# Kernel tuning notes

Hardware: AMD Instinct MI355X
Metric: run time of the kernel (lower is better)

## Reference

```python
import jax, jax.numpy as jnp
import numpy as np


def _segsum(x):
    """Stable segment-sum. x: (..., l) -> (..., l, l) lower-triangular sums."""
    l = x.shape[-1]
    cs = jnp.cumsum(x, axis=-1)
    seg = cs[..., :, None] - cs[..., None, :]
    mask = jnp.tril(jnp.ones((l, l), dtype=bool))
    return jnp.where(mask, seg, -jnp.inf)


def setup_inputs() -> dict:
    key = jax.random.key(0)
    kx, ka, kb, kc = jax.random.split(key, 4)
    b, s, h, p, n = 4, 8192, 32, 64, 16
    X = jax.random.normal(kx, (b, s, h, p), dtype=jnp.float32)
    # negative A for realistic decaying SSM dynamics / numerical safety
    A = -jnp.abs(jax.random.normal(ka, (b, s, h), dtype=jnp.float32)) * 0.5
    B = jax.random.normal(kb, (b, s, h, n), dtype=jnp.float32)
    C = jax.random.normal(kc, (b, s, h, n), dtype=jnp.float32)
    return {"X": X, "A": A, "B": B, "C": C, "block_len": 64}


def reference(X, A, B, C, block_len):
    b, s, h, p = X.shape
    n = B.shape[-1]
    c = s // block_len
    l = block_len
    # chunk: (b, c, l, ...)
    Xb = X.reshape(b, c, l, h, p)
    Bb = B.reshape(b, c, l, h, n)
    Cb = C.reshape(b, c, l, h, n)
    Ab = A.reshape(b, c, l, h).transpose(0, 3, 1, 2)  # (b, h, c, l)
    A_cumsum = jnp.cumsum(Ab, axis=-1)                # (b, h, c, l)

    # 1) intra-chunk (diagonal) output
    L = jnp.exp(_segsum(Ab))                          # (b, h, c, l, l)
    Y_diag = jnp.einsum("bclhn,bcshn,bhcls,bcshp->bclhp", Cb, Bb, L, Xb)

    # 2) intra-chunk states (chunk-final state contribution)
    decay_states = jnp.exp(A_cumsum[..., -1:] - A_cumsum)   # (b, h, c, l)
    states = jnp.einsum("bclhn,bhcl,bclhp->bchpn", Bb, decay_states, Xb)

    # 3) inter-chunk recurrence (zero initial states)
    A_last = A_cumsum[..., -1]                        # (b, h, c)
    decay_chunk = jnp.exp(_segsum(jnp.pad(A_last, ((0, 0), (0, 0), (1, 0)))))  # (b,h,c+1,c+1)
    states = jnp.concatenate([jnp.zeros_like(states[:, :1]), states], axis=1)  # (b,c+1,h,p,n)
    new_states = jnp.einsum("bhzc,bchpn->bzhpn", decay_chunk, states)
    states = new_states[:, :-1]                       # states entering each chunk

    # 4) state -> output (off-diagonal)
    state_decay_out = jnp.exp(A_cumsum)               # (b, h, c, l)
    Y_off = jnp.einsum("bclhn,bchpn,bhcl->bclhp", Cb, states, state_decay_out)

    Y = (Y_diag + Y_off).reshape(b, s, h, p)
    return Y
```

## Files before the change

kernel.cpp:

```cpp
#include <hip/hip_runtime.h>

#define BB 4
#define SS 8192
#define HH 32
#define PP 64
#define NN 16
#define LL 64
#define CC 128
#define SEG 4
#define NSEG (CC / SEG)
#define NCHAIN (BB * HH)
#define NSEGT (NCHAIN * NSEG)

typedef __attribute__((ext_vector_type(8))) short bf16x8;
typedef __attribute__((ext_vector_type(4))) float f32x4;

__device__ inline short f2bf(float f) {
    unsigned u = __builtin_bit_cast(unsigned, f);
    u = (u + 0x7FFFu + ((u >> 16) & 1u)) >> 16;
    return (short)u;
}

__global__ __launch_bounds__(256) void k1_carries(
    const float* __restrict__ X, const float* __restrict__ A,
    const float* __restrict__ B, float* __restrict__ carry,
    float* __restrict__ segd)
{
    int seg = blockIdx.x;
    int chain = seg >> 5;
    int kseg = seg & (NSEG - 1);
    int h = chain & (HH - 1);
    int b = chain >> 5;
    int tid = threadIdx.x;
    int w = tid >> 6, l = tid & 63, g = l >> 4, lr = l & 15;

    __shared__ float Bs[2][LL][17];
    __shared__ float csL[2][LL];
    __shared__ float wls[2][LL];

    float P[4] = {0.f, 0.f, 0.f, 0.f};
    float asum = 0.f;
    float xr[16]; float4 br; float ar = 0.f;

    int c0 = kseg * SEG;

    auto LOADS = [&](int c) {
        size_t row0 = (size_t)b * SS + (size_t)c * LL;
        const float* Xp = X + (row0 * HH + h) * PP;
        const float* Bp = B + (row0 * HH + h) * NN;
        const float* Ap = A + row0 * HH + h;
#pragma unroll
        for (int kt = 0; kt < 2; ++kt)
#pragma unroll
            for (int e = 0; e < 8; ++e)
                xr[kt * 8 + e] = Xp[(size_t)(kt * 32 + g * 8 + e) * (HH * PP) + 16 * w + lr];
        br = *(const float4*)(Bp + (size_t)(tid >> 2) * (HH * NN) + (tid & 3) * 4);
        if (tid < 64) ar = Ap[(size_t)tid * HH];
    };

    auto WRITE = [&](int q1) {
        if (tid < 64) {
            float x = ar;
#pragma unroll
            for (int d = 1; d < 64; d <<= 1) {
                float t = __shfl_up(x, d, 64);
                if (tid >= d) x += t;
            }
            csL[q1][tid] = x;
            float al2 = __shfl(x, 63, 64);
            wls[q1][tid] = __expf(al2 - x);
        }
        int r = tid >> 2, qq = tid & 3;
        Bs[q1][r][qq * 4 + 0] = br.x;
        Bs[q1][r][qq * 4 + 1] = br.y;
        Bs[q1][r][qq * 4 + 2] = br.z;
        Bs[q1][r][qq * 4 + 3] = br.w;
    };

    LOADS(c0);
    WRITE(0);
    __syncthreads();

    for (int cc = 0; cc < SEG; ++cc) {
        int q = cc & 1;
        bf16x8 xf0, xf1;
#pragma unroll
        for (int e = 0; e < 8; ++e) { xf0[e] = f2bf(xr[e]); xf1[e] = f2bf(xr[8 + e]); }
        if (cc + 1 < SEG) LOADS(c0 + cc + 1);

        bf16x8 bt[2];
#pragma unroll
        for (int kt = 0; kt < 2; ++kt) {
            bf16x8 t;
#pragma unroll
            for (int e = 0; e < 8; ++e) {
                int ll2 = kt * 32 + g * 8 + e;
                t[e] = f2bf(Bs[q][ll2][lr] * wls[q][ll2]);
            }
            bt[kt] = t;
        }
        f32x4 st = __builtin_amdgcn_mfma_f32_16x16x32_bf16(bt[0], xf0, (f32x4)0.f, 0, 0, 0);
        st = __builtin_amdgcn_mfma_f32_16x16x32_bf16(bt[1], xf1, st, 0, 0, 0);

        float alast = csL[q][LL - 1];
        float ea = __expf(alast);
#pragma unroll
        for (int r = 0; r < 4; ++r) P[r] = ea * P[r] + st[r];
        asum += alast;

        if (cc + 1 < SEG) WRITE(q ^ 1);
        __syncthreads();
    }

    float4 pv = {P[0], P[1], P[2], P[3]};
    *(float4*)(carry + (size_t)seg * (PP * NN) + (16 * w + lr) * NN + 4 * g) = pv;
    if (tid == 0) segd[seg] = asum;
}

__global__ __launch_bounds__(256) void k2_scan(
    const float* __restrict__ carry, const float* __restrict__ segd,
    float* __restrict__ pin)
{
    int chain = blockIdx.x >> 2;
    int t = ((blockIdx.x & 3) << 8) + threadIdx.x;
    const float* cb = carry + (size_t)chain * NSEG * (PP * NN) + t;
    float* pb = pin + (size_t)chain * NSEG * (PP * NN) + t;
    const float* as = segd + chain * NSEG;
    float P = 0.f;
    for (int k0 = 0; k0 < NSEG; k0 += 8) {
        float s[8], av[8], o[8];
#pragma unroll
        for (int u = 0; u < 8; ++u) s[u] = cb[(size_t)(k0 + u) * (PP * NN)];
#pragma unroll
        for (int u = 0; u < 8; ++u) av[u] = as[k0 + u];
#pragma unroll
        for (int u = 0; u < 8; ++u) { o[u] = P; P = __expf(av[u]) * P + s[u]; }
#pragma unroll
        for (int u = 0; u < 8; ++u) pb[(size_t)(k0 + u) * (PP * NN)] = o[u];
    }
}

__global__ __launch_bounds__(256) void k3_y(
    const float* __restrict__ X, const float* __restrict__ A,
    const float* __restrict__ Bm, const float* __restrict__ Cm,
    const float* __restrict__ pin, float* __restrict__ Y)
{
    int seg = blockIdx.x;
    int chain = seg >> 5;
    int kseg = seg & (NSEG - 1);
    int h = chain & (HH - 1);
    int b = chain >> 5;
    int tid = threadIdx.x;
    int w = tid >> 6, l = tid & 63, g = l >> 4, lr = l & 15;

    __shared__ short XTF[2][8 * 64 * 8];
    __shared__ short ScF[8 * 64 * 8];
    __shared__ float Bs[2][LL][17];
    __shared__ short PT16[2][NN * 68];
    __shared__ float csL[2][LL];
    __shared__ float wls[2][LL];

    ((bf16x8*)ScF)[tid] = (bf16x8)0;
    ((bf16x8*)ScF)[tid + 256] = (bf16x8)0;

    float4 pv = *(const float4*)(pin + (size_t)seg * (PP * NN) + (16 * w + lr) * NN + 4 * g);
    float P[4] = {pv.x, pv.y, pv.z, pv.w};

    float xr[16]; float4 br, cr0, cr1; float ar = 0.f;
    bf16x8 caw;

    int c0 = kseg * SEG;

    auto LOADS = [&](int c) {
        size_t row0 = (size_t)b * SS + (size_t)c * LL;
        const float* Xp = X + (row0 * HH + h) * PP;
        const float* Bp = Bm + (row0 * HH + h) * NN;
        const float* Cp = Cm + (row0 * HH + h) * NN;
        const float* Ap = A + row0 * HH + h;
#pragma unroll
        for (int si = 0; si < 2; ++si) {
            int s = tid + si * 256;
            int sl = s & 63, pt = (s >> 6) & 3, kt = s >> 8;
            int pp2 = pt * 16 + (sl & 15);
            int k0 = kt * 32 + (sl >> 4) * 8;
#pragma unroll
            for (int e = 0; e < 8; ++e)
                xr[si * 8 + e] = Xp[(size_t)(k0 + e) * (HH * PP) + pp2];
        }
        br = *(const float4*)(Bp + (size_t)(tid >> 2) * (HH * NN) + (tid & 3) * 4);
        if (g < 2) {
            const float* crp = Cp + (size_t)(16 * w + lr) * (HH * NN) + g * 8;
            cr0 = *(const float4*)crp;
            cr1 = *(const float4*)(crp + 4);
        }
        if (tid < 64) ar = Ap[(size_t)tid * HH];
    };

    auto WRITE = [&](int q1) {
        if (tid < 64) {
            float x = ar;
#pragma unroll
            for (int d = 1; d < 64; d <<= 1) {
                float t = __shfl_up(x, d, 64);
                if (tid >= d) x += t;
            }
            csL[q1][tid] = x;
            float al2 = __shfl(x, 63, 64);
            wls[q1][tid] = __expf(al2 - x);
        }
        {
            int r = tid >> 2, qq = tid & 3;
            Bs[q1][r][qq * 4 + 0] = br.x;
            Bs[q1][r][qq * 4 + 1] = br.y;
            Bs[q1][r][qq * 4 + 2] = br.z;
            Bs[q1][r][qq * 4 + 3] = br.w;
        }
#pragma unroll
        for (int si = 0; si < 2; ++si) {
            int s = tid + si * 256;
            bf16x8 xb;
#pragma unroll
            for (int e = 0; e < 8; ++e) xb[e] = f2bf(xr[si * 8 + e]);
            ((bf16x8*)(XTF[q1]))[s] = xb;
        }
#pragma unroll
        for (int r = 0; r < 4; ++r)
            PT16[q1][(4 * g + r) * 68 + 16 * w + lr] = f2bf(P[r]);
        bf16x8 t = (bf16x8)0;
        if (g < 2) {
            t[0] = f2bf(cr0.x); t[1] = f2bf(cr0.y); t[2] = f2bf(cr0.z); t[3] = f2bf(cr0.w);
            t[4] = f2bf(cr1.x); t[5] = f2bf(cr1.y); t[6] = f2bf(cr1.z); t[7] = f2bf(cr1.w);
        }
        caw = t;
    };

    LOADS(c0);
    WRITE(0);
    __syncthreads();

    for (int cc = 0; cc < SEG; ++cc) {
        int q = cc & 1;
        if (cc + 1 < SEG) LOADS(c0 + cc + 1);

        float alast = csL[q][LL - 1];
        float cs_i[4], ei[4];
        int ib = 16 * w + 4 * g;
#pragma unroll
        for (int r = 0; r < 4; ++r) { cs_i[r] = csL[q][ib + r]; ei[r] = __expf(cs_i[r]); }

        bf16x8 pf[4];
#pragma unroll
        for (int pt = 0; pt < 4; ++pt) {
            bf16x8 t = (bf16x8)0;
            if (g < 2) {
#pragma unroll
                for (int e = 0; e < 8; ++e)
                    t[e] = PT16[q][(g * 8 + e) * 68 + pt * 16 + lr];
            }
            pf[pt] = t;
        }
        bf16x8 bt[2];
#pragma unroll
        for (int kt = 0; kt < 2; ++kt) {
            bf16x8 t;
#pragma unroll
            for (int e = 0; e < 8; ++e) {
                int ll2 = kt * 32 + g * 8 + e;
                t[e] = f2bf(Bs[q][ll2][lr] * wls[q][ll2]);
            }
            bt[kt] = t;
        }

        for (int jt = 0; jt <= w; ++jt) {
            bf16x8 bw = (bf16x8)0;
            if (g < 2) {
#pragma unroll
                for (int e = 0; e < 8; ++e)
                    bw[e] = f2bf(Bs[q][jt * 16 + lr][g * 8 + e]);
            }
            f32x4 sr = __builtin_amdgcn_mfma_f32_16x16x32_bf16(caw, bw, (f32x4)0.f, 0, 0, 0);
            int j = jt * 16 + lr;
            float csj = csL[q][j];
            int kt2 = j >> 5;
            int flb = 16 * ((j >> 3) & 3);
#pragma unroll
            for (int r = 0; r < 4; ++r) {
                int i15 = g * 4 + r;
                int i = 16 * w + i15;
                float v = (j <= i) ? sr[r] * __expf(cs_i[r] - csj) : 0.f;
                ScF[((w * 2 + kt2) * 64 + i15 + flb) * 8 + (j & 7)] = f2bf(v);
            }
        }

        f32x4 acc[4];
#pragma unroll
        for (int pt = 0; pt < 4; ++pt)
            acc[pt] = __builtin_amdgcn_mfma_f32_16x16x32_bf16(caw, pf[pt], (f32x4)0.f, 0, 0, 0);
#pragma unroll
        for (int pt = 0; pt < 4; ++pt)
#pragma unroll
            for (int r = 0; r < 4; ++r) acc[pt][r] *= ei[r];

        int kts = (w >= 2) ? 2 : 1;
        for (int kt = 0; kt < kts; ++kt) {
            bf16x8 af = ((bf16x8*)ScF)[(w * 2 + kt) * 64 + l];
#pragma unroll
            for (int pt = 0; pt < 4; ++pt) {
                bf16x8 xf = ((bf16x8*)(XTF[q]))[(kt * 4 + pt) * 64 + l];
                acc[pt] = __builtin_amdgcn_mfma_f32_16x16x32_bf16(af, xf, acc[pt], 0, 0, 0);
            }
        }

        f32x4 st = (f32x4)0.f;
#pragma unroll
        for (int kt = 0; kt < 2; ++kt) {
            bf16x8 xf = ((bf16x8*)(XTF[q]))[(kt * 4 + w) * 64 + l];
            st = __builtin_amdgcn_mfma_f32_16x16x32_bf16(bt[kt], xf, st, 0, 0, 0);
        }
        float ea = __expf(alast);
#pragma unroll
        for (int r = 0; r < 4; ++r) P[r] = ea * P[r] + st[r];

        {
            size_t row0 = (size_t)b * SS + (size_t)(c0 + cc) * LL;
            float* Yp = Y + (row0 * HH + h) * PP;
#pragma unroll
            for (int pt = 0; pt < 4; ++pt)
#pragma unroll
                for (int r = 0; r < 4; ++r)
                    Yp[(size_t)(16 * w + 4 * g + r) * (HH * PP) + pt * 16 + lr] = acc[pt][r];
        }

        if (cc + 1 < SEG) WRITE(q ^ 1);
        __syncthreads();
    }
}

extern "C" void kernel_launch(void* const* d_in, const int* in_sizes, int n_in,
                              void* d_out, int out_size, void* d_ws, size_t ws_size,
                              hipStream_t stream)
{
    const float* X = (const float*)d_in[0];
    const float* A = (const float*)d_in[1];
    const float* B = (const float*)d_in[2];
    const float* C = (const float*)d_in[3];
    float* Y = (float*)d_out;

    float* carry = (float*)d_ws;
    float* pin   = carry + (size_t)NSEGT * (PP * NN);
    float* segd  = pin   + (size_t)NSEGT * (PP * NN);

    dim3 blk(256);
    k1_carries<<<dim3(NSEGT), blk, 0, stream>>>(X, A, B, carry, segd);
    k2_scan<<<dim3(NCHAIN * 4), blk, 0, stream>>>(carry, segd, pin);
    k3_y<<<dim3(NSEGT), blk, 0, stream>>>(X, A, B, C, pin, Y);
}
```

Measured before the change: 286.4 us.

## Parallelize output kernel per chunk using stored intra-segment partial states

Result: faster. 275.9 us (-3.7%).

```diff
diff --git a/kernel.cpp b/kernel.cpp
--- a/kernel.cpp
+++ b/kernel.cpp
@@ -11,8 +11,10 @@
 #define NSEG (CC / SEG)
 #define NCHAIN (BB * HH)
 #define NSEGT (NCHAIN * NSEG)
+#define NCHT (NCHAIN * CC)
 
 typedef __attribute__((ext_vector_type(8))) short bf16x8;
+typedef __attribute__((ext_vector_type(4))) short bf16x4;
 typedef __attribute__((ext_vector_type(4))) float f32x4;
 
 __device__ inline short f2bf(float f) {
@@ -24,7 +26,8 @@
 __global__ __launch_bounds__(256) void k1_carries(
     const float* __restrict__ X, const float* __restrict__ A,
     const float* __restrict__ B, float* __restrict__ carry,
-    float* __restrict__ segd)
+    float* __restrict__ segd, float* __restrict__ ploc,
+    float* __restrict__ dsum)
 {
     int seg = blockIdx.x;
     int chain = seg >> 5;
@@ -43,6 +46,7 @@
     float xr[16]; float4 br; float ar = 0.f;
 
     int c0 = kseg * SEG;
+    int pnoff = (16 * w + lr) * NN + 4 * g;
 
     auto LOADS = [&](int c) {
         size_t row0 = (size_t)b * SS + (size_t)c * LL;
@@ -83,6 +87,11 @@
 
     for (int cc = 0; cc < SEG; ++cc) {
         int q = cc & 1;
+        if (cc > 0) {
+            float4 pv = {P[0], P[1], P[2], P[3]};
+            *(float4*)(ploc + (size_t)(chain * CC + c0 + cc) * (PP * NN) + pnoff) = pv;
+            if (tid == 0) dsum[chain * CC + c0 + cc] = asum;
+        }
         bf16x8 xf0, xf1;
 #pragma unroll
         for (int e = 0; e < 8; ++e) { xf0[e] = f2bf(xr[e]); xf1[e] = f2bf(xr[8 + e]); }
@@ -113,7 +122,7 @@
     }
 
     float4 pv = {P[0], P[1], P[2], P[3]};
-    *(float4*)(carry + (size_t)seg * (PP * NN) + (16 * w + lr) * NN + 4 * g) = pv;
+    *(float4*)(carry + (size_t)seg * (PP * NN) + pnoff) = pv;
     if (tid == 0) segd[seg] = asum;
 }
 
@@ -143,197 +152,153 @@
 __global__ __launch_bounds__(256) void k3_y(
     const float* __restrict__ X, const float* __restrict__ A,
     const float* __restrict__ Bm, const float* __restrict__ Cm,
-    const float* __restrict__ pin, float* __restrict__ Y)
+    const float* __restrict__ pin, const float* __restrict__ ploc,
+    const float* __restrict__ dsum, float* __restrict__ Y)
 {
-    int seg = blockIdx.x;
-    int chain = seg >> 5;
-    int kseg = seg & (NSEG - 1);
-    int h = chain & (HH - 1);
-    int b = chain >> 5;
+    int blk = blockIdx.x;
+    int h = blk & (HH - 1);
+    int c = (blk >> 5) & (CC - 1);
+    int b = blk >> 12;
     int tid = threadIdx.x;
     int w = tid >> 6, l = tid & 63, g = l >> 4, lr = l & 15;
-
-    __shared__ short XTF[2][8 * 64 * 8];
+    int chain = b * HH + h;
+    int seg = chain * NSEG + (c >> 2);
+
+    __shared__ short XTF[8 * 64 * 8];
     __shared__ short ScF[8 * 64 * 8];
-    __shared__ float Bs[2][LL][17];
-    __shared__ short PT16[2][NN * 68];
-    __shared__ float csL[2][LL];
-    __shared__ float wls[2][LL];
+    __shared__ short BsF[4 * 64 * 8];
+    __shared__ short PF[4 * 64 * 8];
+    __shared__ float csL[LL];
+
+    size_t row0 = (size_t)b * SS + (size_t)c * LL;
+    const float* Xp = X + (row0 * HH + h) * PP;
+    const float* Bp = Bm + (row0 * HH + h) * NN;
+    const float* Cp = Cm + (row0 * HH + h) * NN;
+    const float* Ap = A + row0 * HH + h;
+    float* Yp = Y + (row0 * HH + h) * PP;
+
+    float xr[16];
+#pragma unroll
+    for (int si = 0; si < 2; ++si) {
+        int k0 = si * 32 + g * 8;
+#pragma unroll
+        for (int e = 0; e < 8; ++e)
+            xr[si * 8 + e] = Xp[(size_t)(k0 + e) * (HH * PP) + 16 * w + lr];
+    }
+    int r = tid >> 2, q = tid & 3;
+    float4 br = *(const float4*)(Bp + (size_t)r * (HH * NN) + q * 4);
+    float4 cr0 = {0,0,0,0}, cr1 = {0,0,0,0};
+    if (g < 2) {
+        const float* crp = Cp + (size_t)(16 * w + lr) * (HH * NN) + g * 8;
+        cr0 = *(const float4*)crp;
+        cr1 = *(const float4*)(crp + 4);
+    }
+    float ar = 0.f;
+    if (tid < 64) ar = Ap[(size_t)tid * HH];
+    int pnoff = (16 * w + lr) * NN + 4 * g;
+    float4 pinv = *(const float4*)(pin + (size_t)seg * (PP * NN) + pnoff);
+    float P4[4];
+    if ((c & (SEG - 1)) == 0) {
+        P4[0] = pinv.x; P4[1] = pinv.y; P4[2] = pinv.z; P4[3] = pinv.w;
+    } else {
+        float4 plv = *(const float4*)(ploc + (size_t)(chain * CC + c) * (PP * NN) + pnoff);
+        float ed = __expf(dsum[chain * CC + c]);
+        P4[0] = ed * pinv.x + plv.x;
+        P4[1] = ed * pinv.y + plv.y;
+        P4[2] = ed * pinv.z + plv.z;
+        P4[3] = ed * pinv.w + plv.w;
+    }
 
     ((bf16x8*)ScF)[tid] = (bf16x8)0;
     ((bf16x8*)ScF)[tid + 256] = (bf16x8)0;
-
-    float4 pv = *(const float4*)(pin + (size_t)seg * (PP * NN) + (16 * w + lr) * NN + 4 * g);
-    float P[4] = {pv.x, pv.y, pv.z, pv.w};
-
-    float xr[16]; float4 br, cr0, cr1; float ar = 0.f;
-    bf16x8 caw;
-
-    int c0 = kseg * SEG;
-
-    auto LOADS = [&](int c) {
-        size_t row0 = (size_t)b * SS + (size_t)c * LL;
-        const float* Xp = X + (row0 * HH + h) * PP;
-        const float* Bp = Bm + (row0 * HH + h) * NN;
-        const float* Cp = Cm + (row0 * HH + h) * NN;
-        const float* Ap = A + row0 * HH + h;
-#pragma unroll
-        for (int si = 0; si < 2; ++si) {
-            int s = tid + si * 256;
-            int sl = s & 63, pt = (s >> 6) & 3, kt = s >> 8;
-            int pp2 = pt * 16 + (sl & 15);
-            int k0 = kt * 32 + (sl >> 4) * 8;
-#pragma unroll
-            for (int e = 0; e < 8; ++e)
-                xr[si * 8 + e] = Xp[(size_t)(k0 + e) * (HH * PP) + pp2];
-        }
-        br = *(const float4*)(Bp + (size_t)(tid >> 2) * (HH * NN) + (tid & 3) * 4);
-        if (g < 2) {
-            const float* crp = Cp + (size_t)(16 * w + lr) * (HH * NN) + g * 8;
-            cr0 = *(const float4*)crp;
-            cr1 = *(const float4*)(crp + 4);
-        }
-        if (tid < 64) ar = Ap[(size_t)tid * HH];
-    };
-
-    auto WRITE = [&](int q1) {
-        if (tid < 64) {
-            float x = ar;
-#pragma unroll
-            for (int d = 1; d < 64; d <<= 1) {
-                float t = __shfl_up(x, d, 64);
-                if (tid >= d) x += t;
-            }
-            csL[q1][tid] = x;
-            float al2 = __shfl(x, 63, 64);
-            wls[q1][tid] = __expf(al2 - x);
-        }
-        {
-            int r = tid >> 2, qq = tid & 3;
-            Bs[q1][r][qq * 4 + 0] = br.x;
-            Bs[q1][r][qq * 4 + 1] = br.y;
-            Bs[q1][r][qq * 4 + 2] = br.z;
-            Bs[q1][r][qq * 4 + 3] = br.w;
-        }
-#pragma unroll
-        for (int si = 0; si < 2; ++si) {
-            int s = tid + si * 256;
-            bf16x8 xb;
-#pragma unroll
-            for (int e = 0; e < 8; ++e) xb[e] = f2bf(xr[si * 8 + e]);
-            ((bf16x8*)(XTF[q1]))[s] = xb;
-        }
-#pragma unroll
-        for (int r = 0; r < 4; ++r)
-            PT16[q1][(4 * g + r) * 68 + 16 * w + lr] = f2bf(P[r]);
-        bf16x8 t = (bf16x8)0;
-        if (g < 2) {
-            t[0] = f2bf(cr0.x); t[1] = f2bf(cr0.y); t[2] = f2bf(cr0.z); t[3] = f2bf(cr0.w);
-            t[4] = f2bf(cr1.x); t[5] = f2bf(cr1.y); t[6] = f2bf(cr1.z); t[7] = f2bf(cr1.w);
-        }
-        caw = t;
-    };
-
-    LOADS(c0);
-    WRITE(0);
+    if (tid < 128)
+        ((bf16x8*)PF)[(tid >> 5) * 64 + 32 + (tid & 31)] = (bf16x8)0;
+
+#pragma unroll
+    for (int si = 0; si < 2; ++si) {
+        bf16x8 xb;
+#pragma unroll
+        for (int e = 0; e < 8; ++e) xb[e] = f2bf(xr[si * 8 + e]);
+        ((bf16x8*)XTF)[tid + si * 256] = xb;
+    }
+    {
+        int fl = (r & 15) + 16 * (q >> 1);
+        int jt = r >> 4;
+        bf16x4 bb = { f2bf(br.x), f2bf(br.y), f2bf(br.z), f2bf(br.w) };
+        ((bf16x4*)BsF)[(jt * 64 + fl) * 2 + (q & 1)] = bb;
+        int zt = tid >> 6, zu = (tid >> 1) & 31, zv = tid & 1;
+        ((bf16x4*)BsF)[(zt * 64 + 32 + zu) * 2 + zv] = (bf16x4)0;
+    }
+#pragma unroll
+    for (int rr = 0; rr < 4; ++rr) {
+        int n = 4 * g + rr;
+        PF[(w * 64 + (n >> 3) * 16 + lr) * 8 + (n & 7)] = f2bf(P4[rr]);
+    }
+    bf16x8 caw = (bf16x8)0;
+    if (g < 2) {
+        caw[0] = f2bf(cr0.x); caw[1] = f2bf(cr0.y);
+        caw[2] = f2bf(cr0.z); caw[3] = f2bf(cr0.w);
+        caw[4] = f2bf(cr1.x); caw[5] = f2bf(cr1.y);
+        caw[6] = f2bf(cr1.z); caw[7] = f2bf(cr1.w);
+    }
+    if (tid < 64) {
+        float x = ar;
+#pragma unroll
+        for (int d = 1; d < 64; d <<= 1) {
+            float t = __shfl_up(x, d, 64);
+            if (tid >= d) x += t;
+        }
+        csL[tid] = x;
+    }
     __syncthreads();
 
-    for (int cc = 0; cc < SEG; ++cc) {
-        int q = cc & 1;
-        if (cc + 1 < SEG) LOADS(c0 + cc + 1);
-
-        float alast = csL[q][LL - 1];
-        float cs_i[4], ei[4];
-        int ib = 16 * w + 4 * g;
-#pragma unroll
-        for (int r = 0; r < 4; ++r) { cs_i[r] = csL[q][ib + r]; ei[r] = __expf(cs_i[r]); }
-
-        bf16x8 pf[4];
+    float cs_i[4], ei[4];
+    int ib = 16 * w + 4 * g;
+#pragma unroll
+    for (int rr = 0; rr < 4; ++rr) { cs_i[rr] = csL[ib + rr]; ei[rr] = __expf(cs_i[rr]); }
+
+    for (int jt = 0; jt <= w; ++jt) {
+        bf16x8 bw = ((bf16x8*)BsF)[jt * 64 + l];
+        f32x4 sr = __builtin_amdgcn_mfma_f32_16x16x32_bf16(caw, bw, (f32x4)0.f, 0, 0, 0);
+        int j = jt * 16 + lr;
+        float csj = csL[j];
+        int kt2 = j >> 5;
+        int flb = 16 * ((j >> 3) & 3);
+#pragma unroll
+        for (int rr = 0; rr < 4; ++rr) {
+            int i15 = g * 4 + rr;
+            int i = 16 * w + i15;
+            float v = (j <= i) ? sr[rr] * __expf(cs_i[rr] - csj) : 0.f;
+            ScF[((w * 2 + kt2) * 64 + i15 + flb) * 8 + (j & 7)] = f2bf(v);
+        }
+    }
+
+    f32x4 acc[4];
+#pragma unroll
+    for (int pt = 0; pt < 4; ++pt) {
+        bf16x8 pfv = ((bf16x8*)PF)[pt * 64 + l];
+        acc[pt] = __builtin_amdgcn_mfma_f32_16x16x32_bf16(caw, pfv, (f32x4)0.f, 0, 0, 0);
+    }
+#pragma unroll
+    for (int pt = 0; pt < 4; ++pt)
+#pragma unroll
+        for (int rr = 0; rr < 4; ++rr) acc[pt][rr] *= ei[rr];
+
+    int kts = (w >= 2) ? 2 : 1;
+    for (int kt = 0; kt < kts; ++kt) {
+        bf16x8 af = ((bf16x8*)ScF)[(w * 2 + kt) * 64 + l];
 #pragma unroll
         for (int pt = 0; pt < 4; ++pt) {
-            bf16x8 t = (bf16x8)0;
-            if (g < 2) {
-#pragma unroll
-                for (int e = 0; e < 8; ++e)
-                    t[e] = PT16[q][(g * 8 + e) * 68 + pt * 16 + lr];
-            }
-            pf[pt] = t;
-        }
-        bf16x8 bt[2];
-#pragma unroll
-        for (int kt = 0; kt < 2; ++kt) {
-            bf16x8 t;
-#pragma unroll
-            for (int e = 0; e < 8; ++e) {
-                int ll2 = kt * 32 + g * 8 + e;
-                t[e] = f2bf(Bs[q][ll2][lr] * wls[q][ll2]);
-            }
-            bt[kt] = t;
-        }
-
-        for (int jt = 0; jt <= w; ++jt) {
-            bf16x8 bw = (bf16x8)0;
-            if (g < 2) {
-#pragma unroll
-                for (int e = 0; e < 8; ++e)
-                    bw[e] = f2bf(Bs[q][jt * 16 + lr][g * 8 + e]);
-            }
-            f32x4 sr = __builtin_amdgcn_mfma_f32_16x16x32_bf16(caw, bw, (f32x4)0.f, 0, 0, 0);
-            int j = jt * 16 + lr;
-            float csj = csL[q][j];
-            int kt2 = j >> 5;
-            int flb = 16 * ((j >> 3) & 3);
-#pragma unroll
-            for (int r = 0; r < 4; ++r) {
-                int i15 = g * 4 + r;
-                int i = 16 * w + i15;
-                float v = (j <= i) ? sr[r] * __expf(cs_i[r] - csj) : 0.f;
-                ScF[((w * 2 + kt2) * 64 + i15 + flb) * 8 + (j & 7)] = f2bf(v);
-            }
-        }
-
-        f32x4 acc[4];
-#pragma unroll
-        for (int pt = 0; pt < 4; ++pt)
-            acc[pt] = __builtin_amdgcn_mfma_f32_16x16x32_bf16(caw, pf[pt], (f32x4)0.f, 0, 0, 0);
-#pragma unroll
-        for (int pt = 0; pt < 4; ++pt)
-#pragma unroll
-            for (int r = 0; r < 4; ++r) acc[pt][r] *= ei[r];
-
-        int kts = (w >= 2) ? 2 : 1;
-        for (int kt = 0; kt < kts; ++kt) {
-            bf16x8 af = ((bf16x8*)ScF)[(w * 2 + kt) * 64 + l];
-#pragma unroll
-            for (int pt = 0; pt < 4; ++pt) {
-                bf16x8 xf = ((bf16x8*)(XTF[q]))[(kt * 4 + pt) * 64 + l];
-                acc[pt] = __builtin_amdgcn_mfma_f32_16x16x32_bf16(af, xf, acc[pt], 0, 0, 0);
-            }
-        }
-
-        f32x4 st = (f32x4)0.f;
-#pragma unroll
-        for (int kt = 0; kt < 2; ++kt) {
-            bf16x8 xf = ((bf16x8*)(XTF[q]))[(kt * 4 + w) * 64 + l];
-            st = __builtin_amdgcn_mfma_f32_16x16x32_bf16(bt[kt], xf, st, 0, 0, 0);
-        }
-        float ea = __expf(alast);
-#pragma unroll
-        for (int r = 0; r < 4; ++r) P[r] = ea * P[r] + st[r];
-
-        {
-            size_t row0 = (size_t)b * SS + (size_t)(c0 + cc) * LL;
-            float* Yp = Y + (row0 * HH + h) * PP;
-#pragma unroll
-            for (int pt = 0; pt < 4; ++pt)
-#pragma unroll
-                for (int r = 0; r < 4; ++r)
-                    Yp[(size_t)(16 * w + 4 * g + r) * (HH * PP) + pt * 16 + lr] = acc[pt][r];
-        }
-
-        if (cc + 1 < SEG) WRITE(q ^ 1);
-        __syncthreads();
-    }
+            bf16x8 xf = ((bf16x8*)XTF)[(kt * 4 + pt) * 64 + l];
+            acc[pt] = __builtin_amdgcn_mfma_f32_16x16x32_bf16(af, xf, acc[pt], 0, 0, 0);
+        }
+    }
+
+#pragma unroll
+    for (int pt = 0; pt < 4; ++pt)
+#pragma unroll
+        for (int rr = 0; rr < 4; ++rr)
+            Yp[(size_t)(16 * w + 4 * g + rr) * (HH * PP) + pt * 16 + lr] = acc[pt][rr];
 }
 
 extern "C" void kernel_launch(void* const* d_in, const int* in_sizes, int n_in,
@@ -348,10 +313,12 @@
 
     float* carry = (float*)d_ws;
     float* pin   = carry + (size_t)NSEGT * (PP * NN);
-    float* segd  = pin   + (size_t)NSEGT * (PP * NN);
+    float* ploc  = pin   + (size_t)NSEGT * (PP * NN);
+    float* segd  = ploc  + (size_t)NCHT * (PP * NN);
+    float* dsum  = segd  + NSEGT;
 
     dim3 blk(256);
-    k1_carries<<<dim3(NSEGT), blk, 0, stream>>>(X, A, B, carry, segd);
+    k1_carries<<<dim3(NSEGT), blk, 0, stream>>>(X, A, B, carry, segd, ploc, dsum);
     k2_scan<<<dim3(NCHAIN * 4), blk, 0, stream>>>(carry, segd, pin);
-    k3_y<<<dim3(NSEGT), blk, 0, stream>>>(X, A, B, C, pin, Y);
-}
+    k3_y<<<dim3(NCHT), blk, 0, stream>>>(X, A, B, C, pin, ploc, dsum, Y);
+}
```
